# Kernel tuning notes

Measured on AMD Instinct MI355X. Metric: run time of the kernel, lower is better.

The kernel has to match this reference:

```python
import jax, jax.numpy as jnp
import numpy as np

IN_DIM = 1024
HIDDEN = 1024
NUM_HEAD = 16
HEAD_DIM = HIDDEN // NUM_HEAD
B, S = 4, 2048


def setup_inputs() -> dict:
    key = jax.random.key(0)
    ks = jax.random.split(key, 10)
    sc = 1.0 / np.sqrt(IN_DIM)
    inp = {
        "x": jax.random.normal(ks[0], (B, S, IN_DIM), dtype=jnp.float32),
        "mask": jnp.ones((B, 1, 1, S), dtype=jnp.int32),
        "Wq": jax.random.normal(ks[1], (IN_DIM, HIDDEN), dtype=jnp.float32) * sc,
        "bq": jnp.zeros((HIDDEN,), dtype=jnp.float32),
        "Wk": jax.random.normal(ks[2], (IN_DIM, HIDDEN), dtype=jnp.float32) * sc,
        "bk": jnp.zeros((HIDDEN,), dtype=jnp.float32),
        "Wv": jax.random.normal(ks[3], (IN_DIM, HIDDEN), dtype=jnp.float32) * sc,
        "bv": jnp.zeros((HIDDEN,), dtype=jnp.float32),
        "Wo": jax.random.normal(ks[4], (HIDDEN, IN_DIM), dtype=jnp.float32) * sc,
        "bo": jnp.zeros((IN_DIM,), dtype=jnp.float32),
    }
    return inp


def reference(x, mask, Wq, bq, Wk, bk, Wv, bv, Wo, bo):
    Bq, Sq, _ = x.shape
    # projections -> [B, H, S, hd]
    def proj(W, b):
        return (x @ W + b).reshape(Bq, Sq, NUM_HEAD, HEAD_DIM).transpose(0, 2, 1, 3)
    q, k, v = proj(Wq, bq), proj(Wk, bk), proj(Wv, bv)
    scale = 1.0 / jnp.sqrt(jnp.asarray(HEAD_DIM, dtype=x.dtype))
    scores = jnp.einsum("bhqd,bhkd->bhqk", q, k) * scale  # [B,H,S,S]
    scores = jnp.where(mask == 0, jnp.asarray(-1e9, dtype=x.dtype), scores)
    attn = jax.nn.softmax(scores, axis=-1)
    out = jnp.einsum("bhqk,bhkd->bhqd", attn, v)  # [B,H,S,hd]
    out = out.transpose(0, 2, 1, 3).reshape(Bq, Sq, HIDDEN)
    return out @ Wo + bo
```

## Files before the change

### kernel.cpp

```cpp
#include <hip/hip_runtime.h>
#include <hip/hip_bf16.h>
#include <stdint.h>

#define BB_ 4
#define SS_ 2048
#define IND_ 1024
#define HIDD_ 1024
#define NH_ 16
#define HD_ 64

typedef __attribute__((ext_vector_type(8))) short vshort8;
typedef __attribute__((ext_vector_type(4))) short vshort4;
typedef __attribute__((ext_vector_type(4))) float vfloat4;

__device__ __forceinline__ short bf16_of(float f) {
    union { float f; uint32_t u; } v; v.f = f;
    uint32_t r = v.u + 0x7fffu + ((v.u >> 16) & 1u);
    return (short)(r >> 16);
}

__device__ __forceinline__ uint32_t pk_bf16(float lo, float hi) {
    uint32_t r;
    asm("v_cvt_pk_bf16_f32 %0, %1, %2" : "=v"(r) : "v"(lo), "v"(hi));
    return r;
}

typedef const __attribute__((address_space(1))) uint8_t* gas_ptr;
typedef __attribute__((address_space(3))) uint8_t* las_ptr;
__device__ __forceinline__ void gload16(const void* g, void* l) {
    __builtin_amdgcn_global_load_lds((gas_ptr)g, (las_ptr)l, 16, 0, 0);
}

__global__ __launch_bounds__(256) void conv_x(const float* __restrict__ x,
                                              short* __restrict__ xb, int n4) {
    int i = blockIdx.x * 256 + threadIdx.x;
    if (i >= n4) return;
    float4 v = ((const float4*)x)[i];
    vshort4 r;
    r[0] = bf16_of(v.x); r[1] = bf16_of(v.y); r[2] = bf16_of(v.z); r[3] = bf16_of(v.w);
    ((vshort4*)xb)[i] = r;
}

__global__ __launch_bounds__(256) void convT_w4(const float* __restrict__ W0,
                                                const float* __restrict__ W1,
                                                const float* __restrict__ W2,
                                                const float* __restrict__ W3,
                                                short* __restrict__ T0,
                                                short* __restrict__ T1,
                                                short* __restrict__ T2,
                                                short* __restrict__ T3) {
    const float* W = (blockIdx.z == 0) ? W0 : (blockIdx.z == 1) ? W1 : (blockIdx.z == 2) ? W2 : W3;
    short* Wt = (blockIdx.z == 0) ? T0 : (blockIdx.z == 1) ? T1 : (blockIdx.z == 2) ? T2 : T3;
    __shared__ short tile[64][65];
    int k0 = blockIdx.x * 64, n0 = blockIdx.y * 64;
#pragma unroll
    for (int i = 0; i < 16; i++) {
        int idx = i * 256 + threadIdx.x;
        int r = idx >> 6, c = idx & 63;
        tile[c][r] = bf16_of(W[(k0 + r) * 1024 + n0 + c]);
    }
    __syncthreads();
#pragma unroll
    for (int i = 0; i < 16; i++) {
        int idx = i * 256 + threadIdx.x;
        int r = idx >> 6, c = idx & 63;
        Wt[(n0 + r) * 1024 + k0 + c] = tile[r][c];
    }
}

template <int MODE>
__device__ __forceinline__ void gemm_body(const short* __restrict__ A,
                                          const short* __restrict__ Bt,
                                          const float* __restrict__ bias,
                                          void* __restrict__ out, float scale,
                                          short* smem) {
    constexpr int Kd = 1024;
    const int t = threadIdx.x;
    const int w = t >> 6, lane = t & 63;
    const int g = lane >> 4, c = lane & 15;
    const int wm = w >> 1, wn = w & 1;
    const int m0 = blockIdx.x * 128, n0 = blockIdx.y * 128;

    const int row = t >> 2;
    const int colE = (t & 3) * 8;

    const short* ga0 = A + (size_t)(m0 + row) * Kd + colE;
    const short* ga1 = A + (size_t)(m0 + 64 + row) * Kd + colE;
    const short* gb0 = Bt + (size_t)(n0 + row) * Kd + colE;
    const short* gb1 = Bt + (size_t)(n0 + 64 + row) * Kd + colE;

    vfloat4 acc[4][4] = {};

    gload16(ga0, &smem[t * 8]);
    gload16(ga1, &smem[2048 + t * 8]);
    gload16(gb0, &smem[4096 + t * 8]);
    gload16(gb1, &smem[6144 + t * 8]);
    __syncthreads();

    for (int k0 = 0; k0 < Kd; k0 += 32) {
        const int cur = (k0 >> 5) & 1;
        const int nb = (cur ^ 1) * 8192;
        if (k0 + 32 < Kd) {
            gload16(ga0 + k0 + 32, &smem[nb + t * 8]);
            gload16(ga1 + k0 + 32, &smem[nb + 2048 + t * 8]);
            gload16(gb0 + k0 + 32, &smem[nb + 4096 + t * 8]);
            gload16(gb1 + k0 + 32, &smem[nb + 6144 + t * 8]);
        }
        const int cb = cur * 8192;
        vshort8 af[4], bfr[4];
#pragma unroll
        for (int mi = 0; mi < 4; mi++)
            af[mi] = *(const vshort8*)&smem[cb + (wm * 64 + mi * 16 + c) * 32 + g * 8];
#pragma unroll
        for (int ni = 0; ni < 4; ni++)
            bfr[ni] = *(const vshort8*)&smem[cb + 4096 + (wn * 64 + ni * 16 + c) * 32 + g * 8];
#pragma unroll
        for (int mi = 0; mi < 4; mi++)
#pragma unroll
            for (int ni = 0; ni < 4; ni++)
                acc[mi][ni] = __builtin_amdgcn_mfma_f32_16x16x32_bf16(
                    af[mi], bfr[ni], acc[mi][ni], 0, 0, 0);
        __syncthreads();
    }

    if (MODE == 2) {
        short* st = smem;
#pragma unroll
        for (int ni = 0; ni < 4; ni++) {
            const int nl = wn * 64 + ni * 16 + c;
            const float bv = bias[n0 + nl];
            const int sx = (nl & 15) << 3;
#pragma unroll
            for (int mi = 0; mi < 4; mi++) {
#pragma unroll
                for (int r = 0; r < 4; r++) {
                    const int ml = wm * 64 + mi * 16 + g * 4 + r;
                    st[nl * 128 + (ml ^ sx)] = bf16_of((acc[mi][ni][r] + bv) * scale);
                }
            }
        }
        __syncthreads();
        const int nl = t >> 1, hb = (t & 1) * 8;
        const int n = n0 + nl, hh = n >> 6, d = n & 63;
        const int b = m0 >> 11, s0l = m0 & 2047;
        short* dst = (short*)out + (((size_t)(b * 16 + hh)) * 64 + d) * 2048 + s0l + (t & 1) * 64;
        const vshort8* srcrow = (const vshort8*)&st[nl * 128];
#pragma unroll
        for (int j = 0; j < 8; j++)
            ((vshort8*)dst)[j] = srcrow[(hb + j) ^ (nl & 15)];
    } else {
#pragma unroll
        for (int ni = 0; ni < 4; ni++) {
            const int n = n0 + wn * 64 + ni * 16 + c;
            const float bv = bias[n];
#pragma unroll
            for (int mi = 0; mi < 4; mi++) {
#pragma unroll
                for (int r = 0; r < 4; r++) {
                    const int m = m0 + wm * 64 + mi * 16 + g * 4 + r;
                    const float v = (acc[mi][ni][r] + bv) * scale;
                    if (MODE == 0) {
                        const int b = m >> 11, s = m & 2047, h = n >> 6, d = n & 63;
                        ((short*)out)[(((size_t)(b * 16 + h)) * 2048 + s) * 64 + d] = bf16_of(v);
                    } else {
                        ((float*)out)[(size_t)m * 1024 + n] = v;
                    }
                }
            }
        }
    }
}

__global__ __launch_bounds__(256) void gemm_qkv(const short* __restrict__ xb,
                                                const short* __restrict__ Wqt,
                                                const short* __restrict__ Wkt,
                                                const short* __restrict__ Wvt,
                                                const float* __restrict__ bq,
                                                const float* __restrict__ bk,
                                                const float* __restrict__ bv,
                                                short* __restrict__ Qb,
                                                short* __restrict__ Kb,
                                                short* __restrict__ Vtb) {
    __shared__ alignas(16) short smem[16384];
    const int z = blockIdx.z;
    if (z == 2) {
        gemm_body<2>(xb, Wvt, bv, Vtb, 1.0f, smem);
    } else if (z == 1) {
        gemm_body<0>(xb, Wkt, bk, Kb, 1.0f, smem);
    } else {
        gemm_body<0>(xb, Wqt, bq, Qb, 0.125f * 1.4426950408889634f, smem);
    }
}

__global__ __launch_bounds__(256) void gemm_out(const short* __restrict__ A,
                                                const short* __restrict__ Bt,
                                                const float* __restrict__ bias,
                                                float* __restrict__ out) {
    __shared__ alignas(16) short smem[16384];
    gemm_body<1>(A, Bt, bias, out, 1.0f, smem);
}

__device__ __forceinline__ vshort8 lds_frag(const short* base, int row, int off) {
    const int byte = row * 128 + (off ^ ((row & 7) << 4));
    return *(const vshort8*)((const char*)base + byte);
}
__device__ __forceinline__ uint2 lds_frag8B(const short* base, int row, int eoff) {
    const int byte = row * 128 + ((eoff * 2) ^ ((row & 7) << 4));
    return *(const uint2*)((const char*)base + byte);
}
__device__ __forceinline__ void lds_stg(short* base, int row, int e8, vshort8 v) {
    const int byte = row * 128 + ((e8 * 16) ^ ((row & 7) << 4));
    *(vshort8*)((char*)base + byte) = v;
}

__global__ __launch_bounds__(512) void attn_kernel(const short* __restrict__ Q,
                                                   const short* __restrict__ K,
                                                   const short* __restrict__ Vt,
                                                   const int* __restrict__ mask,
                                                   short* __restrict__ Oattn) {
    __shared__ alignas(16) short Kl[2][64 * 64];
    __shared__ alignas(16) short Vl[2][64 * 64];
    const int tid = threadIdx.x, w = tid >> 6, lane = tid & 63;
    const int g = lane >> 4, c = lane & 15;
    const int bh = blockIdx.y, bb = bh >> 4, h = bh & 15;
    const int q0 = blockIdx.x * 256 + w * 32;
    const short* Qb = Q + (size_t)bh * 2048 * 64;
    const short* Kb = K + (size_t)bh * 2048 * 64;
    const short* Vb = Vt + (size_t)bh * 64 * 2048;
    const int* mb = mask + bb * 2048;

    const int srow = tid >> 3, se8 = tid & 7;

    vshort8 qa[2][2];
#pragma unroll
    for (int qt = 0; qt < 2; qt++)
#pragma unroll
        for (int kf = 0; kf < 2; kf++)
            qa[qt][kf] = *(const vshort8*)(Qb + (size_t)(q0 + qt * 16 + c) * 64 + kf * 32 + g * 8);

    vfloat4 o[2][4] = {};
    vfloat4 osum[2] = {};
    const vfloat4 ZF = {0.f, 0.f, 0.f, 0.f};
    vshort8 ONESV;
#pragma unroll
    for (int i = 0; i < 8; i++) ONESV[i] = (short)0x3F80;

    vshort8 rk = *(const vshort8*)(Kb + (size_t)srow * 64 + se8 * 8);
    vshort8 rv = *(const vshort8*)(Vb + (size_t)srow * 2048 + se8 * 8);
    lds_stg(Kl[0], srow, se8, rk);
    lds_stg(Vl[0], srow, se8, rv);
    __syncthreads();

    for (int t = 0; t < 32; t++) {
        const int k0 = t * 64;
        const short* Kc = Kl[t & 1];
        const short* Vc = Vl[t & 1];
        const bool more = (t + 1 < 32);
        if (more) {
            const int kn = k0 + 64;
            rk = *(const vshort8*)(Kb + (size_t)(kn + srow) * 64 + se8 * 8);
            rv = *(const vshort8*)(Vb + (size_t)srow * 2048 + kn + se8 * 8);
        }

        const int mv = mb[k0 + lane];
        const bool allone = __all(mv != 0);

        vshort8 kb[4][2];
#pragma unroll
        for (int kt = 0; kt < 4; kt++) {
            kb[kt][0] = lds_frag(Kc, kt * 16 + c, g * 16);
            kb[kt][1] = lds_frag(Kc, kt * 16 + c, 64 + g * 16);
        }
        vfloat4 s[2][4];
        __builtin_amdgcn_s_setprio(1);
#pragma unroll
        for (int qt = 0; qt < 2; qt++)
#pragma unroll
            for (int kt = 0; kt < 4; kt++) {
                vfloat4 z = __builtin_amdgcn_mfma_f32_16x16x32_bf16(kb[kt][0], qa[qt][0], ZF, 0, 0, 0);
                s[qt][kt] = __builtin_amdgcn_mfma_f32_16x16x32_bf16(kb[kt][1], qa[qt][1], z, 0, 0, 0);
            }
        __builtin_amdgcn_s_setprio(0);

        if (!allone) {
#pragma unroll
            for (int kt = 0; kt < 4; kt++)
#pragma unroll
                for (int r = 0; r < 4; r++) {
                    if (mb[k0 + kt * 16 + g * 4 + r] == 0) {
                        s[0][kt][r] = -3e8f;
                        s[1][kt][r] = -3e8f;
                    }
                }
        }

#pragma unroll
        for (int qt = 0; qt < 2; qt++)
#pragma unroll
            for (int kt = 0; kt < 4; kt++)
#pragma unroll
                for (int r = 0; r < 4; r++)
                    s[qt][kt][r] = exp2f(s[qt][kt][r]);

        __builtin_amdgcn_s_setprio(1);
#pragma unroll
        for (int u = 0; u < 2; u++) {
            union { uint32_t uu[4]; vshort8 v; } Pf[2];
#pragma unroll
            for (int qt = 0; qt < 2; qt++) {
                Pf[qt].uu[0] = pk_bf16(s[qt][2 * u][0], s[qt][2 * u][1]);
                Pf[qt].uu[1] = pk_bf16(s[qt][2 * u][2], s[qt][2 * u][3]);
                Pf[qt].uu[2] = pk_bf16(s[qt][2 * u + 1][0], s[qt][2 * u + 1][1]);
                Pf[qt].uu[3] = pk_bf16(s[qt][2 * u + 1][2], s[qt][2 * u + 1][3]);
            }
            const int e0 = (2 * u) * 16 + g * 4;
            const int e1 = (2 * u + 1) * 16 + g * 4;
#pragma unroll
            for (int dt = 0; dt < 4; dt++) {
                const uint2 x0 = lds_frag8B(Vc, dt * 16 + c, e0);
                const uint2 x1 = lds_frag8B(Vc, dt * 16 + c, e1);
                union { uint32_t uu[4]; vshort8 v; } Vf;
                Vf.uu[0] = x0.x; Vf.uu[1] = x0.y; Vf.uu[2] = x1.x; Vf.uu[3] = x1.y;
                o[0][dt] = __builtin_amdgcn_mfma_f32_16x16x32_bf16(Pf[0].v, Vf.v, o[0][dt], 0, 0, 0);
                o[1][dt] = __builtin_amdgcn_mfma_f32_16x16x32_bf16(Pf[1].v, Vf.v, o[1][dt], 0, 0, 0);
            }
            osum[0] = __builtin_amdgcn_mfma_f32_16x16x32_bf16(Pf[0].v, ONESV, osum[0], 0, 0, 0);
            osum[1] = __builtin_amdgcn_mfma_f32_16x16x32_bf16(Pf[1].v, ONESV, osum[1], 0, 0, 0);
        }
        __builtin_amdgcn_s_setprio(0);

        if (more) {
            lds_stg(Kl[(t + 1) & 1], srow, se8, rk);
            lds_stg(Vl[(t + 1) & 1], srow, se8, rv);
            __syncthreads();
        }
    }

#pragma unroll
    for (int qt = 0; qt < 2; qt++)
#pragma unroll
        for (int r = 0; r < 4; r++) {
            const float inv = 1.0f / osum[qt][r];
            const int q = q0 + qt * 16 + g * 4 + r;
#pragma unroll
            for (int dt = 0; dt < 4; dt++) {
                const float v = o[qt][dt][r] * inv;
                Oattn[((size_t)bb * 2048 + q) * 1024 + h * 64 + dt * 16 + c] = bf16_of(v);
            }
        }
}

extern "C" void kernel_launch(void* const* d_in, const int* in_sizes, int n_in,
                              void* d_out, int out_size, void* d_ws, size_t ws_size,
                              hipStream_t stream) {
    const float* x   = (const float*)d_in[0];
    const int*  mask = (const int*)d_in[1];
    const float* Wq  = (const float*)d_in[2];
    const float* bq  = (const float*)d_in[3];
    const float* Wk  = (const float*)d_in[4];
    const float* bk  = (const float*)d_in[5];
    const float* Wv  = (const float*)d_in[6];
    const float* bv  = (const float*)d_in[7];
    const float* Wo  = (const float*)d_in[8];
    const float* bo  = (const float*)d_in[9];
    float* out = (float*)d_out;

    short* xb  = (short*)d_ws;
    short* Wqt = xb + 8192 * 1024;
    short* Wkt = Wqt + 1024 * 1024;
    short* Wvt = Wkt + 1024 * 1024;
    short* Wot = Wvt + 1024 * 1024;
    short* Qb  = Wot + 1024 * 1024;
    short* Kb  = Qb + 8192 * 1024;
    short* Vb  = Kb + 8192 * 1024;
    short* Vtb = Vb + 8192 * 1024;
    short* att = Vtb + 8192 * 1024;

    conv_x<<<8192, 256, 0, stream>>>(x, xb, 8192 * 1024 / 4);
    convT_w4<<<dim3(16, 16, 4), 256, 0, stream>>>(Wq, Wk, Wv, Wo, Wqt, Wkt, Wvt, Wot);

    gemm_qkv<<<dim3(64, 8, 3), 256, 0, stream>>>(xb, Wqt, Wkt, Wvt, bq, bk, bv, Qb, Kb, Vtb);

    attn_kernel<<<dim3(8, 64), 512, 0, stream>>>(Qb, Kb, Vtb, mask, att);

    gemm_out<<<dim3(64, 8), 256, 0, stream>>>(att, Wot, bo, out);
}
```

Measured before the change: 223.3 us.

## Halve attention query tile per wave to double grid and raise occupancy

```diff
diff --git a/kernel.cpp b/kernel.cpp
--- a/kernel.cpp
+++ b/kernel.cpp
@@ -213,17 +213,17 @@
     *(vshort8*)((char*)base + byte) = v;
 }
 
-__global__ __launch_bounds__(512) void attn_kernel(const short* __restrict__ Q,
-                                                   const short* __restrict__ K,
-                                                   const short* __restrict__ Vt,
-                                                   const int* __restrict__ mask,
-                                                   short* __restrict__ Oattn) {
+__global__ __launch_bounds__(512, 8) void attn_kernel(const short* __restrict__ Q,
+                                                      const short* __restrict__ K,
+                                                      const short* __restrict__ Vt,
+                                                      const int* __restrict__ mask,
+                                                      short* __restrict__ Oattn) {
     __shared__ alignas(16) short Kl[2][64 * 64];
     __shared__ alignas(16) short Vl[2][64 * 64];
     const int tid = threadIdx.x, w = tid >> 6, lane = tid & 63;
     const int g = lane >> 4, c = lane & 15;
     const int bh = blockIdx.y, bb = bh >> 4, h = bh & 15;
-    const int q0 = blockIdx.x * 256 + w * 32;
+    const int q0 = blockIdx.x * 128 + w * 16;
     const short* Qb = Q + (size_t)bh * 2048 * 64;
     const short* Kb = K + (size_t)bh * 2048 * 64;
     const short* Vb = Vt + (size_t)bh * 64 * 2048;
@@ -231,15 +231,13 @@
 
     const int srow = tid >> 3, se8 = tid & 7;
 
-    vshort8 qa[2][2];
-#pragma unroll
-    for (int qt = 0; qt < 2; qt++)
-#pragma unroll
-        for (int kf = 0; kf < 2; kf++)
-            qa[qt][kf] = *(const vshort8*)(Qb + (size_t)(q0 + qt * 16 + c) * 64 + kf * 32 + g * 8);
-
-    vfloat4 o[2][4] = {};
-    vfloat4 osum[2] = {};
+    vshort8 qa[2];
+#pragma unroll
+    for (int kf = 0; kf < 2; kf++)
+        qa[kf] = *(const vshort8*)(Qb + (size_t)(q0 + c) * 64 + kf * 32 + g * 8);
+
+    vfloat4 o[4] = {};
+    vfloat4 osum = {};
     const vfloat4 ZF = {0.f, 0.f, 0.f, 0.f};
     vshort8 ONESV;
 #pragma unroll
@@ -265,54 +263,40 @@
         const int mv = mb[k0 + lane];
         const bool allone = __all(mv != 0);
 
-        vshort8 kb[4][2];
+        vfloat4 s[4];
+        __builtin_amdgcn_s_setprio(1);
 #pragma unroll
         for (int kt = 0; kt < 4; kt++) {
-            kb[kt][0] = lds_frag(Kc, kt * 16 + c, g * 16);
-            kb[kt][1] = lds_frag(Kc, kt * 16 + c, 64 + g * 16);
-        }
-        vfloat4 s[2][4];
+            vshort8 kb0 = lds_frag(Kc, kt * 16 + c, g * 16);
+            vshort8 kb1 = lds_frag(Kc, kt * 16 + c, 64 + g * 16);
+            vfloat4 z = __builtin_amdgcn_mfma_f32_16x16x32_bf16(kb0, qa[0], ZF, 0, 0, 0);
+            s[kt] = __builtin_amdgcn_mfma_f32_16x16x32_bf16(kb1, qa[1], z, 0, 0, 0);
+        }
+        __builtin_amdgcn_s_setprio(0);
+
+        if (!allone) {
+#pragma unroll
+            for (int kt = 0; kt < 4; kt++)
+#pragma unroll
+                for (int r = 0; r < 4; r++) {
+                    if (mb[k0 + kt * 16 + g * 4 + r] == 0) s[kt][r] = -3e8f;
+                }
+        }
+
+#pragma unroll
+        for (int kt = 0; kt < 4; kt++)
+#pragma unroll
+            for (int r = 0; r < 4; r++)
+                s[kt][r] = exp2f(s[kt][r]);
+
         __builtin_amdgcn_s_setprio(1);
 #pragma unroll
-        for (int qt = 0; qt < 2; qt++)
-#pragma unroll
-            for (int kt = 0; kt < 4; kt++) {
-                vfloat4 z = __builtin_amdgcn_mfma_f32_16x16x32_bf16(kb[kt][0], qa[qt][0], ZF, 0, 0, 0);
-                s[qt][kt] = __builtin_amdgcn_mfma_f32_16x16x32_bf16(kb[kt][1], qa[qt][1], z, 0, 0, 0);
-            }
-        __builtin_amdgcn_s_setprio(0);
-
-        if (!allone) {
-#pragma unroll
-            for (int kt = 0; kt < 4; kt++)
-#pragma unroll
-                for (int r = 0; r < 4; r++) {
-                    if (mb[k0 + kt * 16 + g * 4 + r] == 0) {
-                        s[0][kt][r] = -3e8f;
-                        s[1][kt][r] = -3e8f;
-                    }
-                }
-        }
-
-#pragma unroll
-        for (int qt = 0; qt < 2; qt++)
-#pragma unroll
-            for (int kt = 0; kt < 4; kt++)
-#pragma unroll
-                for (int r = 0; r < 4; r++)
-                    s[qt][kt][r] = exp2f(s[qt][kt][r]);
-
-        __builtin_amdgcn_s_setprio(1);
-#pragma unroll
         for (int u = 0; u < 2; u++) {
-            union { uint32_t uu[4]; vshort8 v; } Pf[2];
-#pragma unroll
-            for (int qt = 0; qt < 2; qt++) {
-                Pf[qt].uu[0] = pk_bf16(s[qt][2 * u][0], s[qt][2 * u][1]);
-                Pf[qt].uu[1] = pk_bf16(s[qt][2 * u][2], s[qt][2 * u][3]);
-                Pf[qt].uu[2] = pk_bf16(s[qt][2 * u + 1][0], s[qt][2 * u + 1][1]);
-                Pf[qt].uu[3] = pk_bf16(s[qt][2 * u + 1][2], s[qt][2 * u + 1][3]);
-            }
+            union { uint32_t uu[4]; vshort8 v; } Pf;
+            Pf.uu[0] = pk_bf16(s[2 * u][0], s[2 * u][1]);
+            Pf.uu[1] = pk_bf16(s[2 * u][2], s[2 * u][3]);
+            Pf.uu[2] = pk_bf16(s[2 * u + 1][0], s[2 * u + 1][1]);
+            Pf.uu[3] = pk_bf16(s[2 * u + 1][2], s[2 * u + 1][3]);
             const int e0 = (2 * u) * 16 + g * 4;
             const int e1 = (2 * u + 1) * 16 + g * 4;
 #pragma unroll
@@ -321,11 +305,9 @@
                 const uint2 x1 = lds_frag8B(Vc, dt * 16 + c, e1);
                 union { uint32_t uu[4]; vshort8 v; } Vf;
                 Vf.uu[0] = x0.x; Vf.uu[1] = x0.y; Vf.uu[2] = x1.x; Vf.uu[3] = x1.y;
-                o[0][dt] = __builtin_amdgcn_mfma_f32_16x16x32_bf16(Pf[0].v, Vf.v, o[0][dt], 0, 0, 0);
-                o[1][dt] = __builtin_amdgcn_mfma_f32_16x16x32_bf16(Pf[1].v, Vf.v, o[1][dt], 0, 0, 0);
+                o[dt] = __builtin_amdgcn_mfma_f32_16x16x32_bf16(Pf.v, Vf.v, o[dt], 0, 0, 0);
             }
-            osum[0] = __builtin_amdgcn_mfma_f32_16x16x32_bf16(Pf[0].v, ONESV, osum[0], 0, 0, 0);
-            osum[1] = __builtin_amdgcn_mfma_f32_16x16x32_bf16(Pf[1].v, ONESV, osum[1], 0, 0, 0);
+            osum = __builtin_amdgcn_mfma_f32_16x16x32_bf16(Pf.v, ONESV, osum, 0, 0, 0);
         }
         __builtin_amdgcn_s_setprio(0);
 
@@ -337,17 +319,15 @@
     }
 
 #pragma unroll
-    for (int qt = 0; qt < 2; qt++)
-#pragma unroll
-        for (int r = 0; r < 4; r++) {
-            const float inv = 1.0f / osum[qt][r];
-            const int q = q0 + qt * 16 + g * 4 + r;
-#pragma unroll
-            for (int dt = 0; dt < 4; dt++) {
-                const float v = o[qt][dt][r] * inv;
-                Oattn[((size_t)bb * 2048 + q) * 1024 + h * 64 + dt * 16 + c] = bf16_of(v);
-            }
-        }
+    for (int r = 0; r < 4; r++) {
+        const float inv = 1.0f / osum[r];
+        const int q = q0 + g * 4 + r;
+#pragma unroll
+        for (int dt = 0; dt < 4; dt++) {
+            const float v = o[dt][r] * inv;
+            Oattn[((size_t)bb * 2048 + q) * 1024 + h * 64 + dt * 16 + c] = bf16_of(v);
+        }
+    }
 }
 
 extern "C" void kernel_launch(void* const* d_in, const int* in_sizes, int n_in,
@@ -381,7 +361,7 @@
 
     gemm_qkv<<<dim3(64, 8, 3), 256, 0, stream>>>(xb, Wqt, Wkt, Wvt, bq, bk, bv, Qb, Kb, Vtb);
 
-    attn_kernel<<<dim3(8, 64), 512, 0, stream>>>(Qb, Kb, Vtb, mask, att);
+    attn_kernel<<<dim3(16, 64), 512, 0, stream>>>(Qb, Kb, Vtb, mask, att);
 
     gemm_out<<<dim3(64, 8), 256, 0, stream>>>(att, Wot, bo, out);
 }
```

Measured after the change: 305.3 us. +36.8%, slower.
